# Kernel tuning notes

Hardware: AMD Instinct MI355X
Metric: run time of the kernel (lower is better)

## Reference

```python
import jax, jax.numpy as jnp
import numpy as np

B, S = 64, 512
VOCAB, D, H, NH = 50000, 256, 256, 4
MAX_DUR = 12.0
SCALE_RATE = 1.0


def setup_inputs() -> dict:
    key = jax.random.key(0)
    ks = jax.random.split(key, 12)
    s = 1.0 / np.sqrt(H)
    inp = {
        "src": jax.random.randint(ks[0], (B, S), 0, VOCAB),
        "input_len": jax.random.randint(ks[1], (B,), 1, S + 1),
        "fix_src": jax.random.uniform(ks[2], (B, S), jnp.float32) * MAX_DUR,
        "emb_table": jax.random.normal(ks[3], (VOCAB, D), jnp.float32) * 0.02,
        "Wi": jax.random.uniform(ks[4], (H, D), jnp.float32, -s, s),
        "bi": jax.random.uniform(ks[5], (H,), jnp.float32, -s, s),
        "Wh": jax.random.uniform(ks[6], (H, NH * H), jnp.float32, -s, s),
        "bh": jax.random.uniform(ks[7], (H,), jnp.float32, -s, s),
        "fc1_W": jax.random.uniform(ks[8], (D, NH * H), jnp.float32, -s, s),
        "fc1_b": jax.random.uniform(ks[9], (D,), jnp.float32, -s, s),
        "fc2_W": jax.random.uniform(ks[10], (2, D), jnp.float32, -s, s),
        "fc2_b": jax.random.uniform(ks[11], (2,), jnp.float32, -s, s),
    }
    return inp


def _forward(src, input_len, fix_src, emb_table, Wi, bi, Wh, bh, fc1_W, fc1_b, fc2_W, fc2_b):
    emb = emb_table[src]                      # [B, S, D]
    offsets = jnp.arange(NH, dtype=emb.dtype) * (MAX_DUR / NH)  # [NH]
    h0 = jnp.zeros((NH, B, H), emb.dtype)

    def step(h, xd):
        x, d = xd                             # x [B,D], d [B]
        hcat = jnp.swapaxes(h, 0, 1).reshape(B, NH * H)
        cand = jnp.tanh(x @ Wi.T + bi + hcat @ Wh.T + bh)        # [B,H]
        g = jax.nn.sigmoid(d[:, None] * SCALE_RATE - offsets)    # [B,NH]
        gt = g.T[:, :, None]                                     # [NH,B,1]
        h_new = gt * cand[None, :, :] + (1.0 - gt) * h           # [NH,B,H]
        out = jnp.swapaxes(h_new, 0, 1).reshape(B, NH * H)
        return h_new, out

    xs = (jnp.swapaxes(emb, 0, 1), fix_src.T)  # [S,B,D], [S,B]
    _, outs = jax.lax.scan(step, h0, xs)       # [S, B, NH*H]
    outs = jnp.swapaxes(outs, 0, 1)            # [B, S, NH*H]
    sel = outs[jnp.arange(B), input_len - 1]   # gather at last valid step, [B, NH*H]
    hid = jnp.tanh(sel @ fc1_W.T + fc1_b)      # [B, D]
    return hid @ fc2_W.T + fc2_b               # [B, 2]


def reference(src, input_len, fix_src, emb_table, Wi, bi, Wh, bh, fc1_W, fc1_b, fc2_W, fc2_b):
    return _forward(src, input_len, fix_src, emb_table, Wi, bi, Wh, bh, fc1_W, fc1_b, fc2_W, fc2_b)
```

## Files before the change

kernel.cpp:

```cpp
#include <hip/hip_runtime.h>
#include <stdint.h>

constexpr int BB = 64;
constexpr int SS = 512;
constexpr int DD = 256;
constexpr int HH = 256;
constexpr int NHH = 4;
constexpr int KK = 1024;

constexpr int TT = 512;

typedef _Float16 f16;
typedef _Float16 f16x2 __attribute__((ext_vector_type(2)));

__device__ inline float dot2p(uint32_t a, uint32_t b, float c) {
  f16x2 av = __builtin_bit_cast(f16x2, a);
  f16x2 bv = __builtin_bit_cast(f16x2, b);
#if defined(__has_builtin)
#if __has_builtin(__builtin_amdgcn_fdot2)
  return __builtin_amdgcn_fdot2(av, bv, c, false);
#else
  return c + (float)av.x * (float)bv.x + (float)av.y * (float)bv.y;
#endif
#else
  return c + (float)av.x * (float)bv.x + (float)av.y * (float)bv.y;
#endif
}

__device__ inline float dot8(uint4 w, uint4 a, float c) {
  c = dot2p(w.x, a.x, c);
  c = dot2p(w.y, a.y, c);
  c = dot2p(w.z, a.z, c);
  c = dot2p(w.w, a.w, c);
  return c;
}

__device__ inline uint32_t pack2(float a, float b) {
  f16x2 v;
  v.x = (f16)a;
  v.y = (f16)b;
  return __builtin_bit_cast(uint32_t, v);
}

__device__ inline float fast_tanh(float x) {
  x = fminf(fmaxf(x, -15.f), 15.f);
  float e = __expf(2.f * x);
  return 1.f - 2.f / (e + 1.f);
}

__global__ void k_pack_wq(const float* __restrict__ Wh, uint4* __restrict__ Wq) {
  int gid = blockIdx.x * blockDim.x + threadIdx.x;
  int p = gid >> 13;
  int m = (gid >> 9) & 15;
  int t = gid & 511;
  int out = t & 255, ch2 = t >> 8;
  int n = out >> 6, o_loc = out & 63;
  const float* s = Wh + (64 * p + o_loc) * KK + 256 * n + 128 * ch2 + 8 * m;
  uint4 w;
  w.x = pack2(s[0], s[1]);
  w.y = pack2(s[2], s[3]);
  w.z = pack2(s[4], s[5]);
  w.w = pack2(s[6], s[7]);
  Wq[gid] = w;
}

__global__ void k_transpose8(const float* __restrict__ src, float* __restrict__ dst,
                             int C, int total) {
  int gid = blockIdx.x * blockDim.x + threadIdx.x;
  if (gid >= total) return;
  int r = gid & 255, c = gid >> 8;
  dst[gid] = src[r * C + c];
}

__global__ __launch_bounds__(256) void k_precompute_u(
    const int* __restrict__ src, const float* __restrict__ emb,
    const float* __restrict__ WiT, const float* __restrict__ bi,
    const float* __restrict__ bh, const int* __restrict__ input_len,
    f16* __restrict__ U) {
  const int row0 = blockIdx.x * 32;
  const int b = row0 >> 9;
  if ((row0 & 511) >= input_len[b]) return;
  __shared__ float xs[32 * 256];
  __shared__ int srcs[32];
  const int tid = threadIdx.x;
  if (tid < 32) srcs[tid] = src[row0 + tid];
  __syncthreads();
  for (int i = tid; i < 32 * 256; i += 256) {
    int r = i >> 8, d = i & 255;
    xs[i] = emb[srcs[r] * DD + d];
  }
  __syncthreads();
  const int o = tid;
  float acc[32];
#pragma unroll
  for (int r = 0; r < 32; ++r) acc[r] = 0.f;
  for (int d0 = 0; d0 < 256; d0 += 8) {
    float w[8];
#pragma unroll
    for (int j = 0; j < 8; ++j) w[j] = WiT[(d0 + j) * 256 + o];
#pragma unroll
    for (int r = 0; r < 32; ++r) {
      const float4* xp = (const float4*)(xs + r * 256 + d0);
      float4 x0 = xp[0], x1 = xp[1];
      acc[r] += x0.x * w[0] + x0.y * w[1] + x0.z * w[2] + x0.w * w[3] +
                x1.x * w[4] + x1.y * w[5] + x1.z * w[6] + x1.w * w[7];
    }
  }
  float bias = bi[o] + bh[o];
#pragma unroll
  for (int r = 0; r < 32; ++r)
    U[(size_t)(row0 + r) * HH + o] = (f16)(acc[r] + bias);
}

__global__ void __attribute__((amdgpu_flat_work_group_size(512, 512),
                               amdgpu_waves_per_eu(2, 2)))
k_recurrence(
    const uint4* __restrict__ Wq, const f16* __restrict__ U,
    const float* __restrict__ fix_src, const int* __restrict__ input_len,
    const float* __restrict__ fc1T, const float* __restrict__ fc1_b,
    const float* __restrict__ fc2_W, const float* __restrict__ fc2_b,
    float* __restrict__ out, uint32_t* __restrict__ Cex,
    float* __restrict__ FPg, int* __restrict__ Flg) {
  __shared__ __align__(16) char arena[61440];
  f16* cbuf = (f16*)arena;
  uint4* cvec = (uint4*)arena;
  float* partials = (float*)(arena + 512);
  float* hbuf = (float*)(arena + 2560);

  const int idx = blockIdx.x;
  const int b = idx & 63;
  const int p = idx >> 6;
  const int t = threadIdx.x;
  const int out_i = t & 255, ch2 = t >> 8;
  const int n = out_i >> 6, o_loc = out_i & 63;

  uint4 w[16];
  {
    const uint4* wp = Wq + (p * 16) * TT + t;
#pragma unroll
    for (int m = 0; m < 16; ++m) {
      const uint4* a = wp + m * TT;
      asm volatile("global_load_dwordx4 %0, %1, off"
                   : "=v"(w[m]) : "v"(a) : "memory");
    }
    asm volatile("s_waitcnt vmcnt(0)" ::: "memory");
  }

  float v0 = 0.f, v1 = 0.f, v2 = 0.f, v3 = 0.f;
  float h = 0.f;

  const int len = input_len[b];
  const f16* Ub = U + (size_t)b * SS * HH;
  const float* fsb = fix_src + b * SS;

  if (t < 64) {
    float c0 = fast_tanh((float)Ub[64 * p + t]);
    f16 chv = (f16)c0;
    cbuf[64 * p + t] = chv;
    uint32_t dwp =
        ((uint32_t)__builtin_bit_cast(unsigned short, chv) << 16) | 1u;
    __hip_atomic_store(&Cex[b * 256 + p * 64 + t], dwp, __ATOMIC_RELAXED,
                       __HIP_MEMORY_SCOPE_AGENT);
  }

#pragma unroll 1
  for (int s = 0; s < len; ++s) {
#pragma unroll
    for (int m = 0; m < 16; ++m)
      asm volatile("" : "+v"(w[m].x), "+v"(w[m].y), "+v"(w[m].z), "+v"(w[m].w));

    const int par = s & 1;
    const uint32_t tag = (uint32_t)((s + 1) & 0xffff);
    const float dval = fsb[s];
    float g = 0.f, gq1 = 0.f, gq2 = 0.f, gq3 = 0.f, ufn = 0.f;

    if (t < 64) {
      int sn = (s + 1 < len) ? (s + 1) : s;
      ufn = (float)Ub[(size_t)sn * HH + 64 * p + t];
      g   = 1.f / (1.f + __expf(0.f - dval));
      gq1 = 1.f / (1.f + __expf(3.f - dval));
      gq2 = 1.f / (1.f + __expf(6.f - dval));
      gq3 = 1.f / (1.f + __expf(9.f - dval));
    } else if (t < 256) {
      g = 1.f / (1.f + __expf((float)(3 * n) - dval));
      int wv = t >> 6;
      int lane = t & 63;
      int q = (p + wv) & 3;
      uint32_t* addr = &Cex[((par * 64 + b) * 4 + q) * 64 + lane];
      uint32_t dw;
      do {
        dw = __hip_atomic_load(addr, __ATOMIC_RELAXED,
                               __HIP_MEMORY_SCOPE_AGENT);
      } while ((dw & 0xffffu) != tag);
      cbuf[64 * q + lane] =
          __builtin_bit_cast(f16, (unsigned short)(dw >> 16));
    }
    __syncthreads();

    float acc = 0.f;
    const uint4* ap = cvec + ch2 * 16;
#pragma unroll
    for (int m = 0; m < 16; ++m) acc = dot8(w[m], ap[m], acc);
    partials[t] = acc;

    if (t < 256) {
      float cown = (float)cbuf[64 * p + o_loc];
      h = g * cown + (1.f - g) * h;
    }
    __syncthreads();

    if (t < 64) {
      float w0 = partials[t]       + partials[256 + t];
      float w1 = partials[64 + t]  + partials[320 + t];
      float w2 = partials[128 + t] + partials[384 + t];
      float w3 = partials[192 + t] + partials[448 + t];
      v0 = g   * w0 + (1.f - g)   * v0;
      v1 = gq1 * w1 + (1.f - gq1) * v1;
      v2 = gq2 * w2 + (1.f - gq2) * v2;
      v3 = gq3 * w3 + (1.f - gq3) * v3;
      float c = fast_tanh(ufn + (v0 + v1 + v2 + v3));
      f16 chv = (f16)c;
      uint32_t dwp =
          ((uint32_t)__builtin_bit_cast(unsigned short, chv) << 16) |
          (uint32_t)((s + 2) & 0xffff);
      __hip_atomic_store(
          &Cex[(((s + 1) & 1) * 64 + b) * 256 + p * 64 + t], dwp,
          __ATOMIC_RELAXED, __HIP_MEMORY_SCOPE_AGENT);
      cbuf[64 * p + t] = chv;
    }
  }

  if (t < 256) hbuf[out_i] = h;
  __syncthreads();
  {
    float acc = 0.f;
#pragma unroll 4
    for (int r = 0; r < 128; ++r) {
      int k_loc = ch2 * 128 + r;
      int n2 = k_loc >> 6, il = k_loc & 63;
      int kg = n2 * 256 + 64 * p + il;
      acc += hbuf[k_loc] * fc1T[(size_t)kg * 256 + out_i];
    }
    partials[t] = acc;
  }
  __syncthreads();
  if (t < 256) FPg[(b * 4 + p) * 256 + out_i] =
      partials[out_i] + partials[256 + out_i];
  __syncthreads();
  if (t == 0)
    __hip_atomic_store(&Flg[b * 4 + p], 0x5A5A5A5A, __ATOMIC_RELEASE,
                       __HIP_MEMORY_SCOPE_AGENT);
  if (p != 0) return;
  if (t < 4 && t > 0) {
    while (__hip_atomic_load(&Flg[b * 4 + t], __ATOMIC_ACQUIRE,
                             __HIP_MEMORY_SCOPE_AGENT) != 0x5A5A5A5A) {
    }
  }
  __syncthreads();
  if (t < 256) {
    float pre = fc1_b[t];
#pragma unroll
    for (int q = 0; q < 4; ++q)
      pre += __hip_atomic_load(&FPg[(b * 4 + q) * 256 + t], __ATOMIC_RELAXED,
                               __HIP_MEMORY_SCOPE_AGENT);
    hbuf[t] = fast_tanh(pre);
  }
  __syncthreads();
  if (t < 64) {
    float p0 = 0.f, p1 = 0.f;
    for (int oi = t; oi < 256; oi += 64) {
      float hh = hbuf[oi];
      p0 += hh * fc2_W[oi];
      p1 += hh * fc2_W[256 + oi];
    }
#pragma unroll
    for (int off = 32; off; off >>= 1) {
      p0 += __shfl_down(p0, off);
      p1 += __shfl_down(p1, off);
    }
    if (t == 0) {
      out[b * 2 + 0] = p0 + fc2_b[0];
      out[b * 2 + 1] = p1 + fc2_b[1];
    }
  }
}

extern "C" void kernel_launch(void* const* d_in, const int* in_sizes, int n_in,
                              void* d_out, int out_size, void* d_ws, size_t ws_size,
                              hipStream_t stream) {
  const int* src = (const int*)d_in[0];
  const int* input_len = (const int*)d_in[1];
  const float* fix_src = (const float*)d_in[2];
  const float* emb = (const float*)d_in[3];
  const float* Wi = (const float*)d_in[4];
  const float* bi = (const float*)d_in[5];
  const float* Wh = (const float*)d_in[6];
  const float* bh = (const float*)d_in[7];
  const float* fc1_W = (const float*)d_in[8];
  const float* fc1_b = (const float*)d_in[9];
  const float* fc2_W = (const float*)d_in[10];
  const float* fc2_b = (const float*)d_in[11];
  float* out = (float*)d_out;

  char* ws = (char*)d_ws;
  uint4* Wq = (uint4*)(ws);
  float* WiT = (float*)(ws + (512ull << 10));
  float* fc1T = (float*)(ws + (768ull << 10));
  f16* U = (f16*)(ws + (1792ull << 10));
  uint32_t* Cex = (uint32_t*)(ws + (18176ull << 10));
  float* FPg = (float*)(ws + (18304ull << 10));
  int* Flg = (int*)(ws + (18560ull << 10));
  const size_t needed = (18561ull << 10);
  if (ws_size < needed) return;

  k_pack_wq<<<128, 256, 0, stream>>>(Wh, Wq);
  k_transpose8<<<(65536 + 255) / 256, 256, 0, stream>>>(Wi, WiT, 256, 65536);
  k_transpose8<<<(262144 + 255) / 256, 256, 0, stream>>>(fc1_W, fc1T, 1024, 262144);
  k_precompute_u<<<BB * SS / 32, 256, 0, stream>>>(src, emb, WiT, bi, bh,
                                                   input_len, U);
  k_recurrence<<<BB * 4, TT, 0, stream>>>(Wq, U, fix_src, input_len, fc1T,
                                          fc1_b, fc2_W, fc2_b, out, Cex, FPg,
                                          Flg);
}
```

Measured before the change: 777.6 us.

## Compute input projection with fp16 MFMA instead of scalar FP32 FMAs

Replaces the scalar FP32 input-projection kernel with an MFMA 16x16x32 f16 kernel. Embedding rows are staged in LDS as fp16 with an XOR swizzle, and Wi is converted to fp16 rather than transposed. This targets the ALU cost of the precompute stage. It adds fp16 rounding of the embeddings and Wi, so accuracy may shift slightly, and the sequential recurrence kernel still dominates total time.

Result: faster. 719.9 us (-7.4%).

```diff
diff --git a/kernel.cpp b/kernel.cpp
--- a/kernel.cpp
+++ b/kernel.cpp
@@ -12,6 +12,8 @@
 
 typedef _Float16 f16;
 typedef _Float16 f16x2 __attribute__((ext_vector_type(2)));
+typedef _Float16 half8 __attribute__((ext_vector_type(8)));
+typedef float f32x4 __attribute__((ext_vector_type(4)));
 
 __device__ inline float dot2p(uint32_t a, uint32_t b, float c) {
   f16x2 av = __builtin_bit_cast(f16x2, a);
@@ -72,44 +74,59 @@
   dst[gid] = src[r * C + c];
 }
 
-__global__ __launch_bounds__(256) void k_precompute_u(
+__global__ void k_cvt_f16(const float* __restrict__ src, f16* __restrict__ dst,
+                          int total) {
+  int gid = blockIdx.x * blockDim.x + threadIdx.x;
+  if (gid >= total) return;
+  dst[gid] = (f16)src[gid];
+}
+
+__global__ __launch_bounds__(256) void k_u_mfma(
     const int* __restrict__ src, const float* __restrict__ emb,
-    const float* __restrict__ WiT, const float* __restrict__ bi,
+    const f16* __restrict__ wif, const float* __restrict__ bi,
     const float* __restrict__ bh, const int* __restrict__ input_len,
     f16* __restrict__ U) {
-  const int row0 = blockIdx.x * 32;
+  __shared__ __align__(16) char xls[32768];
+  const int row0 = blockIdx.x * 64;
   const int b = row0 >> 9;
   if ((row0 & 511) >= input_len[b]) return;
-  __shared__ float xs[32 * 256];
-  __shared__ int srcs[32];
-  const int tid = threadIdx.x;
-  if (tid < 32) srcs[tid] = src[row0 + tid];
-  __syncthreads();
-  for (int i = tid; i < 32 * 256; i += 256) {
-    int r = i >> 8, d = i & 255;
-    xs[i] = emb[srcs[r] * DD + d];
-  }
-  __syncthreads();
-  const int o = tid;
-  float acc[32];
-#pragma unroll
-  for (int r = 0; r < 32; ++r) acc[r] = 0.f;
-  for (int d0 = 0; d0 < 256; d0 += 8) {
-    float w[8];
-#pragma unroll
-    for (int j = 0; j < 8; ++j) w[j] = WiT[(d0 + j) * 256 + o];
-#pragma unroll
-    for (int r = 0; r < 32; ++r) {
-      const float4* xp = (const float4*)(xs + r * 256 + d0);
-      float4 x0 = xp[0], x1 = xp[1];
-      acc[r] += x0.x * w[0] + x0.y * w[1] + x0.z * w[2] + x0.w * w[3] +
-                x1.x * w[4] + x1.y * w[5] + x1.z * w[6] + x1.w * w[7];
-    }
-  }
-  float bias = bi[o] + bh[o];
-#pragma unroll
-  for (int r = 0; r < 32; ++r)
-    U[(size_t)(row0 + r) * HH + o] = (f16)(acc[r] + bias);
+  const int t = threadIdx.x;
+  const int w = t >> 6, l = t & 63;
+
+  for (int rr = 0; rr < 16; ++rr) {
+    int r = w * 16 + rr;
+    int srcid = src[row0 + r];
+    const float4 x = *(const float4*)(emb + (size_t)srcid * DD + l * 4);
+    uint2 dw;
+    dw.x = pack2(x.x, x.y);
+    dw.y = pack2(x.z, x.w);
+    int byte = (r * 512 + l * 8) ^ ((r & 7) << 4);
+    *(uint2*)(xls + byte) = dw;
+  }
+  __syncthreads();
+
+  const int lm = l & 15, lk = l >> 4;
+  const int arow = w * 16 + lm;
+  const int xs = (arow & 7) << 4;
+
+  for (int ct = 0; ct < 16; ++ct) {
+    const int o = ct * 16 + lm;
+    f32x4 acc = {0.f, 0.f, 0.f, 0.f};
+    const f16* bp = wif + (size_t)o * 256 + lk * 8;
+#pragma unroll
+    for (int kt = 0; kt < 8; ++kt) {
+      int ab = (arow * 512 + kt * 64 + lk * 16) ^ xs;
+      half8 af = *(const half8*)(xls + ab);
+      half8 bf = *(const half8*)(bp + kt * 32);
+      acc = __builtin_amdgcn_mfma_f32_16x16x32_f16(af, bf, acc, 0, 0, 0);
+    }
+    float bias = bi[o] + bh[o];
+#pragma unroll
+    for (int reg = 0; reg < 4; ++reg) {
+      int grow = row0 + w * 16 + lk * 4 + reg;
+      U[(size_t)grow * HH + o] = (f16)(acc[reg] + bias);
+    }
+  }
 }
 
 __global__ void __attribute__((amdgpu_flat_work_group_size(512, 512),
@@ -304,7 +321,7 @@
 
   char* ws = (char*)d_ws;
   uint4* Wq = (uint4*)(ws);
-  float* WiT = (float*)(ws + (512ull << 10));
+  f16* wif = (f16*)(ws + (512ull << 10));
   float* fc1T = (float*)(ws + (768ull << 10));
   f16* U = (f16*)(ws + (1792ull << 10));
   uint32_t* Cex = (uint32_t*)(ws + (18176ull << 10));
@@ -314,10 +331,10 @@
   if (ws_size < needed) return;
 
   k_pack_wq<<<128, 256, 0, stream>>>(Wh, Wq);
-  k_transpose8<<<(65536 + 255) / 256, 256, 0, stream>>>(Wi, WiT, 256, 65536);
+  k_cvt_f16<<<(65536 + 255) / 256, 256, 0, stream>>>(Wi, wif, 65536);
   k_transpose8<<<(262144 + 255) / 256, 256, 0, stream>>>(fc1_W, fc1T, 1024, 262144);
-  k_precompute_u<<<BB * SS / 32, 256, 0, stream>>>(src, emb, WiT, bi, bh,
-                                                   input_len, U);
+  k_u_mfma<<<BB * SS / 64, 256, 0, stream>>>(src, emb, wif, bi, bh,
+                                             input_len, U);
   k_recurrence<<<BB * 4, TT, 0, stream>>>(Wq, U, fix_src, input_len, fc1T,
                                           fc1_b, fc2_W, fc2_b, out, Cex, FPg,
                                           Flg);
```
